# Optimization experiments

Hardware: AMD Instinct MI355X
Metric: run time of the kernel (lower is better)

The kernel has to match this reference:

```python
import jax, jax.numpy as jnp
import numpy as np

DIM = 1024
HEADS = 16
B, N = 4, 1024

def setup_inputs() -> dict:
    key = jax.random.key(0)
    k1, k2, k3 = jax.random.split(key, 3)
    x = jax.random.normal(k1, (B, N, DIM), dtype=jnp.float32)
    # xavier-uniform-ish init scale
    Wqkv = jax.random.normal(k2, (3 * DIM, DIM), dtype=jnp.float32) * (1.0 / np.sqrt(DIM))
    bqkv = jnp.zeros((3 * DIM,), dtype=jnp.float32)
    W1 = jax.random.normal(k3, (DIM, DIM), dtype=jnp.float32) * (1.0 / np.sqrt(DIM))
    b1 = jnp.zeros((DIM,), dtype=jnp.float32)
    return {"x": x, "Wqkv": Wqkv, "bqkv": bqkv, "W1": W1, "b1": b1}

def reference(x, Wqkv, bqkv, W1, b1):
    b, n, dim = x.shape
    h = HEADS
    d = dim // h
    scale = dim ** (-0.5)  # NOTE: module scales by full dim, not head dim
    qkv = x @ Wqkv.T + bqkv  # [b, n, 3*dim]
    qkv = qkv.reshape(b, n, 3, h, d)
    q = jnp.transpose(qkv[:, :, 0], (0, 2, 1, 3))  # [b, h, n, d]
    k = jnp.transpose(qkv[:, :, 1], (0, 2, 1, 3))
    v = jnp.transpose(qkv[:, :, 2], (0, 2, 1, 3))
    dots = jnp.einsum('bhid,bhjd->bhij', q, k) * scale
    attn = jax.nn.softmax(dots, axis=-1)
    out = jnp.einsum('bhij,bhjd->bhid', attn, v)
    out = jnp.transpose(out, (0, 2, 1, 3)).reshape(b, n, dim)
    out = out @ W1.T + b1
    return out
```

## Files before the change

### kernel.cpp

```cpp
#include <hip/hip_runtime.h>
#include <cmath>

typedef __bf16 bf16;
typedef __bf16 bf16x8 __attribute__((ext_vector_type(8)));
typedef __bf16 bf16x4 __attribute__((ext_vector_type(4)));
typedef float f32x4 __attribute__((ext_vector_type(4)));

#define MFMA16(a, b, c) __builtin_amdgcn_mfma_f32_16x16x32_bf16(a, b, c, 0, 0, 0)

__device__ __forceinline__ void load_lds16(const void* g, void* l) {
    __builtin_amdgcn_global_load_lds(
        (const __attribute__((address_space(1))) void*)g,
        (__attribute__((address_space(3))) void*)l, 16, 0, 0);
}

__device__ __forceinline__ bf16x8 load8(const bf16* p) { return *(const bf16x8*)p; }
__device__ __forceinline__ bf16x8 load8(const float* p) {
    float4 f0 = *(const float4*)p;
    float4 f1 = *(const float4*)(p + 4);
    bf16x8 r;
    r[0] = (bf16)f0.x; r[1] = (bf16)f0.y; r[2] = (bf16)f0.z; r[3] = (bf16)f0.w;
    r[4] = (bf16)f1.x; r[5] = (bf16)f1.y; r[6] = (bf16)f1.z; r[7] = (bf16)f1.w;
    return r;
}

__global__ __launch_bounds__(256) void cvt3(
    const float* __restrict__ s0, bf16* __restrict__ d0, int n0,
    const float* __restrict__ s1, bf16* __restrict__ d1, int n1,
    const float* __restrict__ s2, bf16* __restrict__ d2, int n2)
{
    int i = blockIdx.x * 256 + threadIdx.x;
    const float* s; bf16* d; int base;
    if (i < n0)                { s = s0; d = d0; base = i; }
    else if (i < n0 + n1)      { s = s1; d = d1; base = i - n0; }
    else if (i < n0 + n1 + n2) { s = s2; d = d2; base = i - n0 - n1; }
    else return;
    *(bf16x8*)(d + (size_t)base * 8) = load8(s + (size_t)base * 8);
}

template <int EPI, typename TB, int BN>
__global__ __launch_bounds__(256) void gemm_bt(
    const bf16* __restrict__ A, const TB* __restrict__ Bm,
    const float* __restrict__ bias,
    bf16* __restrict__ qo, bf16* __restrict__ ko, bf16* __restrict__ vto,
    float* __restrict__ C, int M, int N, int K)
{
    constexpr int WN = BN / 2;
    constexpr int JN = WN / 16;
    constexpr int SLOTS = (128 + BN) * 8;

    __shared__ bf16 As[128 * 64];
    __shared__ bf16 Bs[BN * 64];

    const int tid = threadIdx.x;
    const int l   = tid & 63;
    const int w   = tid >> 6;
    const int wm  = w & 1, wn = w >> 1;
    const int l15 = l & 15;
    const int g   = l >> 4;
    const int swz = l15 & 7;
    const int m0  = blockIdx.y * 128;
    const int n0  = blockIdx.x * BN;

    f32x4 acc[4][JN] = {};

    for (int k0 = 0; k0 < K; k0 += 64) {
        __syncthreads();
        #pragma unroll
        for (int it = 0; it < SLOTS / 256; ++it) {
            int s = it * 256 + w * 64 + l;
            if (s < 1024) {
                int row = s >> 3, pc = s & 7;
                int lc  = pc ^ (row & 7);
                load_lds16(A + (size_t)(m0 + row) * K + k0 + lc * 8, &As[s * 8]);
            } else {
                int t = s - 1024;
                int row = t >> 3, pc = t & 7;
                int lc  = pc ^ (row & 7);
                if constexpr (sizeof(TB) == 2) {
                    load_lds16(Bm + (size_t)(n0 + row) * K + k0 + lc * 8, &Bs[t * 8]);
                } else {
                    *(bf16x8*)&Bs[t * 8] = load8(Bm + (size_t)(n0 + row) * K + k0 + lc * 8);
                }
            }
        }
        __syncthreads();
        #pragma unroll
        for (int kk = 0; kk < 64; kk += 32) {
            bf16x8 aF[4], bF[JN];
            #pragma unroll
            for (int i = 0; i < 4; ++i)
                aF[i] = *(const bf16x8*)&As[(wm * 64 + i * 16 + l15) * 64
                                            + ((((kk >> 3) + g) ^ swz) * 8)];
            #pragma unroll
            for (int j = 0; j < JN; ++j)
                bF[j] = *(const bf16x8*)&Bs[(wn * WN + j * 16 + l15) * 64
                                            + ((((kk >> 3) + g) ^ swz) * 8)];
            #pragma unroll
            for (int i = 0; i < 4; ++i)
                #pragma unroll
                for (int j = 0; j < JN; ++j)
                    acc[i][j] = MFMA16(aF[i], bF[j], acc[i][j]);
        }
    }

    #pragma unroll
    for (int j = 0; j < JN; ++j) {
        int gcol = n0 + wn * WN + j * 16 + l15;
        float bv = bias[gcol];
        if (EPI == 0) {
            int which = gcol >> 10;
            int h  = (gcol >> 6) & 15;
            int dd = gcol & 63;
            #pragma unroll
            for (int i = 0; i < 4; ++i) {
                #pragma unroll
                for (int r = 0; r < 4; ++r) {
                    int grow = m0 + wm * 64 + i * 16 + g * 4 + r;
                    int b    = grow >> 10;
                    int npos = grow & 1023;
                    float v  = acc[i][j][r] + bv;
                    size_t bh = (size_t)(b * 16 + h);
                    if (which == 0)
                        qo[(bh * 1024 + npos) * 64 + dd] = (bf16)v;
                    else if (which == 1)
                        ko[(bh * 1024 + npos) * 64 + dd] = (bf16)v;
                    else
                        vto[(bh * 64 + dd) * 1024 + npos] = (bf16)v;
                }
            }
        } else {
            #pragma unroll
            for (int i = 0; i < 4; ++i)
                #pragma unroll
                for (int r = 0; r < 4; ++r) {
                    int grow = m0 + wm * 64 + i * 16 + g * 4 + r;
                    C[(size_t)grow * N + gcol] = acc[i][j][r] + bv;
                }
        }
    }
}

__global__ __launch_bounds__(256) void attn_fused(
    const bf16* __restrict__ qb, const bf16* __restrict__ kb,
    const bf16* __restrict__ vtb, bf16* __restrict__ attn)
{
    __shared__ bf16 Ks[64 * 64];
    __shared__ bf16 Vts[64 * 64];
    __shared__ bf16 Ps[4][16][72];

    const int tid = threadIdx.x;
    const int l   = tid & 63;
    const int w   = tid >> 6;
    const int l15 = l & 15;
    const int g   = l >> 4;
    const int swz = l15 & 7;
    const int bid = blockIdx.x;
    const int bh  = bid & 63;
    const int qc  = bid >> 6;
    const int m0  = qc * 64;

    const bf16* q_bh  = qb  + (size_t)bh * 65536;
    const bf16* k_bh  = kb  + (size_t)bh * 65536;
    const bf16* vt_bh = vtb + (size_t)bh * 65536;

    bf16x8 qf[2];
    #pragma unroll
    for (int kk = 0; kk < 2; ++kk)
        qf[kk] = *(const bf16x8*)(q_bh + (size_t)(m0 + w * 16 + l15) * 64
                                  + kk * 32 + g * 8);

    f32x4 o[4] = {};
    float lsum = 0.f;

    const float C_EXP = 0.04508422f;

    for (int j0 = 0; j0 < 1024; j0 += 64) {
        __syncthreads();
        #pragma unroll
        for (int it = 0; it < 2; ++it) {
            int s   = it * 256 + w * 64 + l;
            int row = s >> 3, pc = s & 7;
            int lc  = pc ^ (row & 7);
            load_lds16(k_bh + (size_t)(j0 + row) * 64 + lc * 8, &Ks[s * 8]);
            load_lds16(vt_bh + (size_t)row * 1024 + j0 + lc * 8, &Vts[s * 8]);
        }
        __syncthreads();

        f32x4 s4[4] = {};
        #pragma unroll
        for (int kk = 0; kk < 2; ++kk) {
            bf16x8 kf[4];
            #pragma unroll
            for (int js = 0; js < 4; ++js)
                kf[js] = *(const bf16x8*)&Ks[(js * 16 + l15) * 64
                                             + (((kk * 4 + g) ^ swz) * 8)];
            #pragma unroll
            for (int js = 0; js < 4; ++js)
                s4[js] = MFMA16(kf[js], qf[kk], s4[js]);
        }

        #pragma unroll
        for (int js = 0; js < 4; ++js) {
            bf16x4 pk;
            float ps = 0.f;
            #pragma unroll
            for (int r = 0; r < 4; ++r) {
                float p = exp2f(s4[js][r] * C_EXP);
                ps += p;
                pk[r] = (bf16)p;
            }
            lsum += ps;
            *(bf16x4*)&Ps[w][l15][js * 16 + g * 4] = pk;
        }
        __syncthreads();

        #pragma unroll
        for (int kk = 0; kk < 2; ++kk) {
            bf16x8 vf[4];
            #pragma unroll
            for (int ns = 0; ns < 4; ++ns)
                vf[ns] = *(const bf16x8*)&Vts[(ns * 16 + l15) * 64
                                              + (((kk * 4 + g) ^ swz) * 8)];
            bf16x8 pf = *(const bf16x8*)&Ps[w][l15][kk * 32 + g * 8];
            #pragma unroll
            for (int ns = 0; ns < 4; ++ns)
                o[ns] = MFMA16(pf, vf[ns], o[ns]);
        }
    }

    float t = lsum;
    t += __shfl_xor(t, 16);
    t += __shfl_xor(t, 32);

    #pragma unroll
    for (int r = 0; r < 4; ++r) {
        float inv = 1.0f / __shfl(t, g * 4 + r);
        int grow = m0 + w * 16 + g * 4 + r;
        size_t obase = ((size_t)(bh >> 4) * 1024 + grow) * 1024 + (bh & 15) * 64;
        #pragma unroll
        for (int ns = 0; ns < 4; ++ns)
            attn[obase + ns * 16 + l15] = (bf16)(o[ns][r] * inv);
    }
}

extern "C" void kernel_launch(void* const* d_in, const int* in_sizes, int n_in,
                              void* d_out, int out_size, void* d_ws, size_t ws_size,
                              hipStream_t stream)
{
    const float* x    = (const float*)d_in[0];
    const float* Wqkv = (const float*)d_in[1];
    const float* bqkv = (const float*)d_in[2];
    const float* W1   = (const float*)d_in[3];
    const float* b1   = (const float*)d_in[4];
    float* out = (float*)d_out;

    const size_t SEG = (size_t)4 * 16 * 1024 * 64;
    bf16* xbf  = (bf16*)d_ws;
    bf16* qb   = xbf + SEG;
    bf16* kb   = qb + SEG;
    bf16* vtb  = kb + SEG;
    bf16* attnb = xbf;
    bf16* wqkvbf = vtb + SEG;
    bf16* w1bf   = wqkvbf + 3145728;

    const bool cw = ws_size >= (size_t)(5 * SEG) * sizeof(bf16);

    const int nx = 524288;
    const int nw = cw ? 393216 : 0;
    const int n1 = cw ? 131072 : 0;
    const int tot = nx + nw + n1;
    cvt3<<<dim3((tot + 255) / 256), 256, 0, stream>>>(
        x, xbf, nx, Wqkv, wqkvbf, nw, W1, w1bf, n1);

    if (cw)
        gemm_bt<0, bf16, 128><<<dim3(24, 32), 256, 0, stream>>>(
            xbf, wqkvbf, bqkv, qb, kb, vtb, nullptr, 4096, 3072, 1024);
    else
        gemm_bt<0, float, 128><<<dim3(24, 32), 256, 0, stream>>>(
            xbf, Wqkv, bqkv, qb, kb, vtb, nullptr, 4096, 3072, 1024);

    attn_fused<<<dim3(1024), 256, 0, stream>>>(qb, kb, vtb, attnb);

    if (cw)
        gemm_bt<1, bf16, 64><<<dim3(16, 32), 256, 0, stream>>>(
            attnb, w1bf, b1, nullptr, nullptr, nullptr, out, 4096, 1024, 1024);
    else
        gemm_bt<1, float, 64><<<dim3(16, 32), 256, 0, stream>>>(
            attnb, W1, b1, nullptr, nullptr, nullptr, out, 4096, 1024, 1024);
}
```

Before: 175.3 us.

## Double-buffer K/V tiles in attention and drop the mid-loop block barrier

The attention kernel now keeps two LDS buffers for K and V^T tiles. The next tile's async global-to-LDS load is issued right after the barrier at the top of each iteration, so the copy can overlap the current tile's MFMA and softmax work. The per-wave P tile is produced and consumed in two 32-column halves inside the PV loop, which removes the second __syncthreads per iteration and shrinks the Ps buffer. MFMA sections are wrapped in s_setprio to favour matrix issue. LDS use roughly doubles for K/V, which may lower occupancy.

```diff
diff --git a/kernel.cpp b/kernel.cpp
--- a/kernel.cpp
+++ b/kernel.cpp
@@ -145,9 +145,9 @@
     const bf16* __restrict__ qb, const bf16* __restrict__ kb,
     const bf16* __restrict__ vtb, bf16* __restrict__ attn)
 {
-    __shared__ bf16 Ks[64 * 64];
-    __shared__ bf16 Vts[64 * 64];
-    __shared__ bf16 Ps[4][16][72];
+    __shared__ bf16 Ks[2][64 * 64];
+    __shared__ bf16 Vts[2][64 * 64];
+    __shared__ bf16 Ps[4][16][40];
 
     const int tid = threadIdx.x;
     const int l   = tid & 63;
@@ -175,17 +175,23 @@
 
     const float C_EXP = 0.04508422f;
 
-    for (int j0 = 0; j0 < 1024; j0 += 64) {
-        __syncthreads();
+    auto stage = [&](int buf, int j0) {
         #pragma unroll
         for (int it = 0; it < 2; ++it) {
             int s   = it * 256 + w * 64 + l;
             int row = s >> 3, pc = s & 7;
             int lc  = pc ^ (row & 7);
-            load_lds16(k_bh + (size_t)(j0 + row) * 64 + lc * 8, &Ks[s * 8]);
-            load_lds16(vt_bh + (size_t)row * 1024 + j0 + lc * 8, &Vts[s * 8]);
-        }
+            load_lds16(k_bh + (size_t)(j0 + row) * 64 + lc * 8, &Ks[buf][s * 8]);
+            load_lds16(vt_bh + (size_t)row * 1024 + j0 + lc * 8, &Vts[buf][s * 8]);
+        }
+    };
+
+    stage(0, 0);
+
+    for (int t = 0; t < 16; ++t) {
+        const int c = t & 1;
         __syncthreads();
+        if (t < 15) stage(c ^ 1, (t + 1) * 64);
 
         f32x4 s4[4] = {};
         #pragma unroll
@@ -193,39 +199,42 @@
             bf16x8 kf[4];
             #pragma unroll
             for (int js = 0; js < 4; ++js)
-                kf[js] = *(const bf16x8*)&Ks[(js * 16 + l15) * 64
-                                             + (((kk * 4 + g) ^ swz) * 8)];
+                kf[js] = *(const bf16x8*)&Ks[c][(js * 16 + l15) * 64
+                                                + (((kk * 4 + g) ^ swz) * 8)];
+            __builtin_amdgcn_s_setprio(1);
             #pragma unroll
             for (int js = 0; js < 4; ++js)
                 s4[js] = MFMA16(kf[js], qf[kk], s4[js]);
-        }
-
-        #pragma unroll
-        for (int js = 0; js < 4; ++js) {
-            bf16x4 pk;
-            float ps = 0.f;
-            #pragma unroll
-            for (int r = 0; r < 4; ++r) {
-                float p = exp2f(s4[js][r] * C_EXP);
-                ps += p;
-                pk[r] = (bf16)p;
+            __builtin_amdgcn_s_setprio(0);
+        }
+
+        #pragma unroll
+        for (int h = 0; h < 2; ++h) {
+            #pragma unroll
+            for (int jsl = 0; jsl < 2; ++jsl) {
+                int js = h * 2 + jsl;
+                bf16x4 pk;
+                float ps = 0.f;
+                #pragma unroll
+                for (int r = 0; r < 4; ++r) {
+                    float p = exp2f(s4[js][r] * C_EXP);
+                    ps += p;
+                    pk[r] = (bf16)p;
+                }
+                lsum += ps;
+                *(bf16x4*)&Ps[w][l15][jsl * 16 + g * 4] = pk;
             }
-            lsum += ps;
-            *(bf16x4*)&Ps[w][l15][js * 16 + g * 4] = pk;
-        }
-        __syncthreads();
-
-        #pragma unroll
-        for (int kk = 0; kk < 2; ++kk) {
             bf16x8 vf[4];
             #pragma unroll
             for (int ns = 0; ns < 4; ++ns)
-                vf[ns] = *(const bf16x8*)&Vts[(ns * 16 + l15) * 64
-                                              + (((kk * 4 + g) ^ swz) * 8)];
-            bf16x8 pf = *(const bf16x8*)&Ps[w][l15][kk * 32 + g * 8];
+                vf[ns] = *(const bf16x8*)&Vts[c][(ns * 16 + l15) * 64
+                                                 + (((h * 4 + g) ^ swz) * 8)];
+            bf16x8 pf = *(const bf16x8*)&Ps[w][l15][g * 8];
+            __builtin_amdgcn_s_setprio(1);
             #pragma unroll
             for (int ns = 0; ns < 4; ++ns)
                 o[ns] = MFMA16(pf, vf[ns], o[ns]);
+            __builtin_amdgcn_s_setprio(0);
         }
     }
 
```

Result: faster. 171.7 us (-2.1%).
